# Optimization experiments

Measured on AMD Instinct MI355X. Metric: run time of the kernel, lower is better.

The kernel has to match this reference:

```python
import jax, jax.numpy as jnp
import numpy as np
from jax import lax

T, H, I, E = 1024, 1024, 512, 16          # tokens, hidden, moe_intermediate, n_routed_experts
TOP_K, N_GROUP, TOPK_GROUP = 4, 4, 2
N_SHARED = 2
I_SHARED = I * N_SHARED                    # shared-expert intermediate size
ROUTED_SCALE = 2.5


def setup_inputs() -> dict:
    key = jax.random.key(0)
    ks = jax.random.split(key, 9)
    s = lambda k, shape, fan: jax.random.normal(k, shape, jnp.float32) * (fan ** -0.5)
    return {
        "hidden_states": jax.random.normal(ks[0], (T, H), jnp.float32),
        "router_w": s(ks[1], (H, E), H),                 # gate: ReplicatedLinear(H, E)
        "e_bias": jax.random.normal(ks[2], (E,), jnp.float32) * 0.01,  # e_score_correction_bias
        "w_gate": s(ks[3], (E, H, I), H),                # routed experts gate_proj
        "w_up": s(ks[4], (E, H, I), H),                  # routed experts up_proj
        "w_down": s(ks[5], (E, I, H), I),                # routed experts down_proj
        "sw_gate": s(ks[6], (H, I_SHARED), H),           # shared experts gate_proj
        "sw_up": s(ks[7], (H, I_SHARED), H),             # shared experts up_proj
        "sw_down": s(ks[8], (I_SHARED, H), I_SHARED),    # shared experts down_proj
    }


def _grouped_topk_sigmoid(logits, e_bias):
    # DeepSeek-V3 'noaux_tc' grouped top-k with sigmoid scoring.
    scores = jax.nn.sigmoid(logits)                      # [T, E]
    sc = scores + e_bias                                 # biased scores for selection only
    g = sc.reshape(-1, N_GROUP, E // N_GROUP)
    group_scores = lax.top_k(g, 2)[0].sum(-1)            # [T, n_group]: sum of top-2 per group
    _, gidx = lax.top_k(group_scores, TOPK_GROUP)        # [T, topk_group]
    gmask = jax.nn.one_hot(gidx, N_GROUP, dtype=sc.dtype).sum(1)  # [T, n_group]
    emask = jnp.repeat(gmask, E // N_GROUP, axis=1)      # [T, E]
    masked = jnp.where(emask > 0, sc, 0.0)               # sigmoid scores are >=0
    _, tidx = lax.top_k(masked, TOP_K)                   # [T, top_k]
    w = jnp.take_along_axis(scores, tidx, axis=1)        # weights use UNbiased scores
    w = w / (w.sum(-1, keepdims=True) + 1e-20)           # norm_topk_prob=True
    # dense combine weights [T, E]
    combine = (jax.nn.one_hot(tidx, E, dtype=w.dtype) * w[..., None]).sum(1)
    return combine


def reference(hidden_states, router_w, e_bias, w_gate, w_up, w_down,
              sw_gate, sw_up, sw_down):
    x = hidden_states                                    # [T, H]
    logits = x @ router_w                                # [T, E]
    combine = _grouped_topk_sigmoid(logits, e_bias)      # [T, E]

    # routed experts: SiLU-gated MLP per expert, dense-over-experts reference
    gp = jnp.einsum('th,ehi->tei', x, w_gate)            # [T, E, I]
    up = jnp.einsum('th,ehi->tei', x, w_up)
    h = jax.nn.silu(gp) * up
    oe = jnp.einsum('tei,eih->teh', h, w_down)           # [T, E, H]
    routed = jnp.einsum('teh,te->th', oe, combine)       # [T, H]

    # shared experts MLP (reduce_results=False path), fp32 path scales routed only
    shared = (jax.nn.silu(x @ sw_gate) * (x @ sw_up)) @ sw_down  # [T, H]
    return routed * ROUTED_SCALE + shared
```

## Files before the change

### kernel.cpp

```cpp
#include <hip/hip_runtime.h>
#include <stdint.h>

#define T_TOK 1024
#define HDIM  1024
#define IDIM  512
#define NEXP  16
#define ISH   1024
#define MAXT128  48
#define HSLOTS   6144

typedef _Float16 f16;
typedef __attribute__((ext_vector_type(8))) _Float16 f16x8;
typedef __attribute__((ext_vector_type(4))) _Float16 f16x4;
typedef __attribute__((ext_vector_type(4))) float    f32x4;

__device__ __forceinline__ void gld16(const void* g, void* l) {
  __builtin_amdgcn_global_load_lds(
      (__attribute__((address_space(1))) void*)(uintptr_t)g,
      (__attribute__((address_space(3))) void*)(uint32_t)(uintptr_t)l,
      16, 0, 0);
}

__device__ __forceinline__ f16x8 ldsfragA(const f16* buf, int row, int lch) {
  int phys = lch ^ (row & 7);
  return *(const f16x8*)(buf + row * 64 + phys * 8);
}

__device__ __forceinline__ f16x8 ldsfragB(const f16* buf, int n, int kc) {
  int c = kc ^ ((n >> 3) & 7);
  return *(const f16x8*)(buf + n * 72 + c * 8);
}

__device__ __forceinline__ void stageB(const float* __restrict__ W, int ldW,
                                       int kt, int n0, f16* __restrict__ Bs,
                                       int nbase, int tid) {
  int p = tid & 31, kg = tid >> 5;
  int n = 2 * p;
  const float* src = W + (size_t)(kt + 8 * kg) * ldW + n0 + n;
  float2 v[8];
#pragma unroll
  for (int r = 0; r < 8; r++) v[r] = *(const float2*)(src + (size_t)r * ldW);
  f16x8 c0, c1;
#pragma unroll
  for (int r = 0; r < 8; r++) { c0[r] = (f16)v[r].x; c1[r] = (f16)v[r].y; }
  int nn = nbase + n;
  int cc = kg ^ ((nn >> 3) & 7);
  *(f16x8*)(Bs + (size_t)nn * 72 + cc * 8) = c0;
  *(f16x8*)(Bs + (size_t)(nn + 1) * 72 + cc * 8) = c1;
}

__global__ __launch_bounds__(256) void router_kernel(
    const float* __restrict__ x, const float* __restrict__ rw, const float* __restrict__ ebias,
    f16* __restrict__ xh, int* __restrict__ topk_i, float* __restrict__ topk_w) {
  int wave = threadIdx.x >> 6, l = threadIdx.x & 63;
  int t = blockIdx.x * 4 + wave;
  float acc[16];
#pragma unroll
  for (int e = 0; e < 16; e++) acc[e] = 0.f;
#pragma unroll
  for (int i = 0; i < 4; i++) {
    int k = i * 256 + l * 4;
    float4 xv = *(const float4*)(x + (size_t)t * HDIM + k);
    f16x4 h = { (f16)xv.x, (f16)xv.y, (f16)xv.z, (f16)xv.w };
    *(f16x4*)(xh + (size_t)t * HDIM + k) = h;
    const float* xp = &xv.x;
#pragma unroll
    for (int j = 0; j < 4; j++) {
      float xj = xp[j];
      const float4* w4 = (const float4*)(rw + (size_t)(k + j) * 16);
#pragma unroll
      for (int q = 0; q < 4; q++) {
        float4 w = w4[q];
        acc[q*4+0] += xj * w.x; acc[q*4+1] += xj * w.y;
        acc[q*4+2] += xj * w.z; acc[q*4+3] += xj * w.w;
      }
    }
  }
#pragma unroll
  for (int off = 32; off >= 1; off >>= 1)
#pragma unroll
    for (int e = 0; e < 16; e++) acc[e] += __shfl_xor(acc[e], off, 64);

  if (l == 0) {
    float s[16], sc[16];
#pragma unroll
    for (int e = 0; e < 16; e++) {
      s[e] = 1.f / (1.f + __expf(-acc[e]));
      sc[e] = s[e] + ebias[e];
    }
    float gs[4];
#pragma unroll
    for (int g = 0; g < 4; g++) {
      float a = -1e30f, b2 = -1e30f;
#pragma unroll
      for (int j = 0; j < 4; j++) {
        float v = sc[g*4 + j];
        if (v > a) { b2 = a; a = v; } else if (v > b2) { b2 = v; }
      }
      gs[g] = a + b2;
    }
    int g1 = 0;
    for (int g = 1; g < 4; g++) if (gs[g] > gs[g1]) g1 = g;
    int g2 = -1;
    for (int g = 0; g < 4; g++) if (g != g1 && (g2 < 0 || gs[g] > gs[g2])) g2 = g;
    float masked[16];
#pragma unroll
    for (int e = 0; e < 16; e++) {
      int g = e >> 2;
      masked[e] = (g == g1 || g == g2) ? sc[e] : 0.0f;
    }
    int idx[4]; float wv[4]; float denom = 1e-20f;
#pragma unroll
    for (int j = 0; j < 4; j++) {
      int best = 0; float bv = masked[0];
      for (int e = 1; e < 16; e++) if (masked[e] > bv) { bv = masked[e]; best = e; }
      idx[j] = best; wv[j] = s[best]; denom += s[best];
      masked[best] = -1e30f;
    }
#pragma unroll
    for (int j = 0; j < 4; j++) {
      topk_i[t * 4 + j] = idx[j];
      topk_w[t * 4 + j] = wv[j] / denom * 2.5f;
    }
  }
}

__global__ __launch_bounds__(1024) void scatter_kernel(
    const int* __restrict__ tki,
    int* __restrict__ tok, int* __restrict__ slotmap,
    int* __restrict__ tile_e, int* __restrict__ tile_srow,
    int* __restrict__ tile_hb, int* __restrict__ ntl) {
  __shared__ int lcnt[NEXP], lpos[NEXP], lbase[NEXP];
  int t = threadIdx.x;
  if (t < NEXP) { lcnt[t] = 0; lpos[t] = 0; }
  __syncthreads();
  int idx[4];
#pragma unroll
  for (int j = 0; j < 4; j++) idx[j] = tki[t*4+j];
#pragma unroll
  for (int j = 0; j < 4; j++) atomicAdd(&lcnt[idx[j]], 1);
  __syncthreads();
  if (t == 0) {
    int total = 0, slots = 0;
    for (int e = 0; e < NEXP; e++) {
      int c = lcnt[e], nt = (c + 127) >> 7;
      lbase[e] = slots;
      for (int j = 0; j < nt; j++) {
        tile_e[total] = e; tile_srow[total] = j * 128; tile_hb[total] = slots + j * 128; total++;
      }
      slots += nt * 128;
    }
    ntl[0] = total;
  }
  __syncthreads();
#pragma unroll
  for (int j = 0; j < 4; j++) {
    int slot = atomicAdd(&lpos[idx[j]], 1);
    tok[idx[j] * T_TOK + slot] = t;
    slotmap[t * 4 + j] = lbase[idx[j]] + slot;
  }
  __syncthreads();
  int e = t >> 6, s = t & 63;
  int c = lcnt[e];
  int top = ((c + 127) >> 7) << 7;
  for (int s2 = c + s; s2 < top; s2 += 64) tok[e * T_TOK + s2] = 0;
}

__device__ __forceinline__ f32x4 mfma16(f16x8 a, f16x8 b, f32x4 c) {
  return __builtin_amdgcn_mfma_f32_16x16x32_f16(a, b, c, 0, 0, 0);
}

__global__ __launch_bounds__(256) void gu_all(
    const f16* __restrict__ xh,
    const float* __restrict__ sg, const float* __restrict__ su, f16* __restrict__ hsh,
    const float* __restrict__ wg, const float* __restrict__ wu, f16* __restrict__ hbuf,
    const int* __restrict__ tile_e, const int* __restrict__ tile_srow,
    const int* __restrict__ tile_hb, const int* __restrict__ ntl,
    const int* __restrict__ tok) {
  int b = blockIdx.x;
  const float *Bg, *Bu; f16* Hdst;
  int e = 0, srow = 0, mbase, n0, N;
  bool gather = (b >= 128);
  if (!gather) {
    Bg = sg; Bu = su; Hdst = hsh; N = ISH;
    mbase = (b >> 4) * 128; n0 = (b & 15) * 64;
  } else {
    int rb = b - 128, by = rb >> 3;
    if (by >= ntl[0]) return;
    e = tile_e[by]; srow = tile_srow[by]; mbase = tile_hb[by];
    size_t bo = (size_t)e * HDIM * IDIM;
    Bg = wg + bo; Bu = wu + bo; Hdst = hbuf; N = IDIM;
    n0 = (rb & 7) * 64;
  }
  const int K = HDIM;

  __shared__ f16 As[128 * 64];
  __shared__ f16 Bgs[64 * 72], Bus[64 * 72];

  int tid = threadIdx.x, lane = tid & 63, wave = tid >> 6;
  int quad = lane >> 4, l15 = lane & 15;
  int r = lane >> 3, p = lane & 7;

  const f16* gbA[4]; f16* lbA[4];
#pragma unroll
  for (int jj = 0; jj < 4; jj++) {
    int j = wave * 4 + jj;
    int kcol = (p ^ r) << 3;
    int row = j * 8 + r;
    int grow = gather ? tok[e * T_TOK + srow + row] : (mbase + row);
    gbA[jj] = xh + (size_t)grow * K + kcol;
    lbA[jj] = (f16*)As + (j << 9);
  }

  int wr = wave >> 1, wc = wave & 1;
  f32x4 zero = {0.f, 0.f, 0.f, 0.f};
  f32x4 aG[4][2], aU[4][2];
#pragma unroll
  for (int mi = 0; mi < 4; mi++)
#pragma unroll
    for (int ni = 0; ni < 2; ni++) { aG[mi][ni] = zero; aU[mi][ni] = zero; }

  for (int kt = 0; kt < K; kt += 64) {
    __syncthreads();
#pragma unroll
    for (int jj = 0; jj < 4; jj++) gld16(gbA[jj] + kt, lbA[jj]);
    stageB(Bg, N, kt, n0, Bgs, 0, tid);
    stageB(Bu, N, kt, n0, Bus, 0, tid);
    __syncthreads();
#pragma unroll
    for (int ks = 0; ks < 2; ks++) {
      int lch = (ks << 2) + quad;
      f16x8 a[4], g[2], u[2];
#pragma unroll
      for (int mi = 0; mi < 4; mi++) a[mi] = ldsfragA(As, 64 * wr + 16 * mi + l15, lch);
#pragma unroll
      for (int ni = 0; ni < 2; ni++) {
        g[ni] = ldsfragB(Bgs, 32 * wc + 16 * ni + l15, lch);
        u[ni] = ldsfragB(Bus, 32 * wc + 16 * ni + l15, lch);
      }
#pragma unroll
      for (int mi = 0; mi < 4; mi++)
#pragma unroll
        for (int ni = 0; ni < 2; ni++) {
          aG[mi][ni] = mfma16(a[mi], g[ni], aG[mi][ni]);
          aU[mi][ni] = mfma16(a[mi], u[ni], aU[mi][ni]);
        }
    }
  }
#pragma unroll
  for (int mi = 0; mi < 4; mi++)
#pragma unroll
    for (int ni = 0; ni < 2; ni++)
#pragma unroll
      for (int rg = 0; rg < 4; rg++) {
        int m = 64 * wr + 16 * mi + (quad << 2) + rg;
        int n = n0 + 32 * wc + 16 * ni + l15;
        float g = aG[mi][ni][rg], u = aU[mi][ni][rg];
        float val = (g / (1.f + __expf(-g))) * u;
        Hdst[(size_t)(mbase + m) * N + n] = (f16)val;
      }
}

__global__ __launch_bounds__(256) void down_all(
    const f16* __restrict__ hsh, const float* __restrict__ sd,
    const f16* __restrict__ hbuf, const float* __restrict__ wd,
    float* __restrict__ out, f16* __restrict__ odown,
    const int* __restrict__ tile_hb, const int* __restrict__ tile_e,
    const int* __restrict__ ntl) {
  int b = blockIdx.x;
  bool routed = (b >= 64);
  const f16* A; const float* B; int K, abase, n0;
  if (!routed) {
    A = hsh; B = sd; K = ISH;
    abase = (b >> 3) * 128; n0 = (b & 7) * 128;
  } else {
    int rb = b - 64, by = rb >> 3;
    if (by >= ntl[0]) return;
    abase = tile_hb[by];
    A = hbuf; B = wd + (size_t)tile_e[by] * IDIM * HDIM; K = IDIM;
    n0 = (rb & 7) * 128;
  }

  __shared__ f16 As[128 * 64];
  __shared__ f16 Bs[128 * 72];

  int tid = threadIdx.x, lane = tid & 63, wave = tid >> 6;
  int quad = lane >> 4, l15 = lane & 15;
  int r = lane >> 3, p = lane & 7;

  const f16* gbA[4]; f16* lbA[4];
#pragma unroll
  for (int jj = 0; jj < 4; jj++) {
    int j = wave * 4 + jj;
    int kcol = (p ^ r) << 3;
    int row = j * 8 + r;
    gbA[jj] = A + (size_t)(abase + row) * K + kcol;
    lbA[jj] = (f16*)As + (j << 9);
  }

  int wr = wave >> 1, wc = wave & 1;
  f32x4 zero = {0.f, 0.f, 0.f, 0.f};
  f32x4 ac[4][4];
#pragma unroll
  for (int mi = 0; mi < 4; mi++)
#pragma unroll
    for (int ni = 0; ni < 4; ni++) ac[mi][ni] = zero;

  for (int kt = 0; kt < K; kt += 64) {
    __syncthreads();
#pragma unroll
    for (int jj = 0; jj < 4; jj++) gld16(gbA[jj] + kt, lbA[jj]);
    stageB(B, HDIM, kt, n0,      Bs, 0,  tid);
    stageB(B, HDIM, kt, n0 + 64, Bs, 64, tid);
    __syncthreads();
#pragma unroll
    for (int ks = 0; ks < 2; ks++) {
      int lch = (ks << 2) + quad;
      f16x8 a[4], bb[4];
#pragma unroll
      for (int mi = 0; mi < 4; mi++) a[mi] = ldsfragA(As, 64 * wr + 16 * mi + l15, lch);
#pragma unroll
      for (int ni = 0; ni < 4; ni++) bb[ni] = ldsfragB(Bs, 64 * wc + 16 * ni + l15, lch);
#pragma unroll
      for (int mi = 0; mi < 4; mi++)
#pragma unroll
        for (int ni = 0; ni < 4; ni++)
          ac[mi][ni] = mfma16(a[mi], bb[ni], ac[mi][ni]);
    }
  }
#pragma unroll
  for (int mi = 0; mi < 4; mi++)
#pragma unroll
    for (int ni = 0; ni < 4; ni++)
#pragma unroll
      for (int rg = 0; rg < 4; rg++) {
        int m = 64 * wr + 16 * mi + (quad << 2) + rg;
        int n = n0 + 64 * wc + 16 * ni + l15;
        if (routed) odown[(size_t)(abase + m) * HDIM + n] = (f16)ac[mi][ni][rg];
        else        out  [(size_t)(abase + m) * HDIM + n] = ac[mi][ni][rg];
      }
}

__global__ __launch_bounds__(256) void combine_kernel(
    const f16* __restrict__ odown, const int* __restrict__ slotmap,
    const float* __restrict__ tkw, float* __restrict__ out) {
  int t = blockIdx.x;
  __shared__ int ss[4]; __shared__ float sw[4];
  if (threadIdx.x < 4) {
    ss[threadIdx.x] = slotmap[t * 4 + threadIdx.x];
    sw[threadIdx.x] = tkw[t * 4 + threadIdx.x];
  }
  __syncthreads();
  int h = threadIdx.x * 4;
  float4 acc = *(const float4*)(out + (size_t)t * HDIM + h);
#pragma unroll
  for (int j = 0; j < 4; j++) {
    f16x4 v = *(const f16x4*)(odown + (size_t)ss[j] * HDIM + h);
    float wj = sw[j];
    acc.x += wj * (float)v[0]; acc.y += wj * (float)v[1];
    acc.z += wj * (float)v[2]; acc.w += wj * (float)v[3];
  }
  *(float4*)(out + (size_t)t * HDIM + h) = acc;
}

extern "C" void kernel_launch(void* const* d_in, const int* in_sizes, int n_in,
                              void* d_out, int out_size, void* d_ws, size_t ws_size,
                              hipStream_t stream) {
  const float* x  = (const float*)d_in[0];
  const float* rw = (const float*)d_in[1];
  const float* eb = (const float*)d_in[2];
  const float* wg = (const float*)d_in[3];
  const float* wu = (const float*)d_in[4];
  const float* wd = (const float*)d_in[5];
  const float* sg = (const float*)d_in[6];
  const float* su = (const float*)d_in[7];
  const float* sd = (const float*)d_in[8];
  float* out = (float*)d_out;
  (void)in_sizes; (void)n_in; (void)out_size; (void)ws_size;

  char* w = (char*)d_ws;
  size_t off = 0;
  auto alloc = [&](size_t b) { void* p = w + off; off = (off + b + 255) & ~(size_t)255; return p; };

  f16* xh   = (f16*)alloc((size_t)T_TOK * HDIM * 2);
  f16* hbuf = (f16*)alloc((size_t)HSLOTS * IDIM * 2);
  f16* hsh  = (f16*)alloc((size_t)T_TOK * ISH * 2);
  f16* odown = (f16*)alloc((size_t)HSLOTS * HDIM * 2);
  int* topk_i = (int*)alloc((size_t)T_TOK * 4 * 4);
  float* topk_w = (float*)alloc((size_t)T_TOK * 4 * 4);
  int* tok  = (int*)alloc((size_t)NEXP * T_TOK * 4);
  int* slotmap = (int*)alloc((size_t)T_TOK * 4 * 4);
  int* tile_e    = (int*)alloc(MAXT128 * 4);
  int* tile_srow = (int*)alloc(MAXT128 * 4);
  int* tile_hb   = (int*)alloc(MAXT128 * 4);
  int* ntl       = (int*)alloc(16);

  router_kernel<<<T_TOK / 4, 256, 0, stream>>>(x, rw, eb, xh, topk_i, topk_w);
  scatter_kernel<<<1, 1024, 0, stream>>>(topk_i, tok, slotmap,
                                         tile_e, tile_srow, tile_hb, ntl);
  gu_all<<<128 + MAXT128 * 8, 256, 0, stream>>>(
      xh, sg, su, hsh, wg, wu, hbuf, tile_e, tile_srow, tile_hb, ntl, tok);
  down_all<<<64 + MAXT128 * 8, 256, 0, stream>>>(
      hsh, sd, hbuf, wd, out, odown, tile_hb, tile_e, ntl);
  combine_kernel<<<T_TOK, 256, 0, stream>>>(odown, slotmap, topk_w, out);
}
```

Before: 228.0 us.

## Double-buffer GEMM K-loop and shrink tiles to raise block count

Both GEMM kernels now prefetch the next K-slice into registers (B, fp32 weights) and a second LDS buffer (A) while the current slice feeds the MFMAs. This overlaps global loads with compute instead of the previous load-sync-compute pattern. It also halves the tile sizes: gate/up goes to 64-row M tiles with matching 64-row expert tiles, and down goes to 64-column N tiles. The aim is to launch more blocks and fill more CUs. In exchange there is more redundant weight traffic per block, and the scheduler must now build two tile lists.

```diff
diff --git a/kernel.cpp b/kernel.cpp
--- a/kernel.cpp
+++ b/kernel.cpp
@@ -6,6 +6,7 @@
 #define IDIM  512
 #define NEXP  16
 #define ISH   1024
+#define MAXT64   96
 #define MAXT128  48
 #define HSLOTS   6144
 
@@ -20,33 +21,36 @@
       (__attribute__((address_space(3))) void*)(uint32_t)(uintptr_t)l,
       16, 0, 0);
 }
+__device__ __forceinline__ void barrier_raw()  { __builtin_amdgcn_s_barrier(); }
+__device__ __forceinline__ void barrier_full() {
+  __builtin_amdgcn_s_waitcnt(0);
+  __builtin_amdgcn_s_barrier();
+}
 
 __device__ __forceinline__ f16x8 ldsfragA(const f16* buf, int row, int lch) {
   int phys = lch ^ (row & 7);
   return *(const f16x8*)(buf + row * 64 + phys * 8);
 }
-
 __device__ __forceinline__ f16x8 ldsfragB(const f16* buf, int n, int kc) {
   int c = kc ^ ((n >> 3) & 7);
   return *(const f16x8*)(buf + n * 72 + c * 8);
 }
-
-__device__ __forceinline__ void stageB(const float* __restrict__ W, int ldW,
-                                       int kt, int n0, f16* __restrict__ Bs,
-                                       int nbase, int tid) {
+__device__ __forceinline__ void loadB(const float* __restrict__ W, int ldW,
+                                      int kt, int n0, int tid, float2 v[8]) {
   int p = tid & 31, kg = tid >> 5;
-  int n = 2 * p;
-  const float* src = W + (size_t)(kt + 8 * kg) * ldW + n0 + n;
-  float2 v[8];
+  const float* src = W + (size_t)(kt + 8 * kg) * ldW + n0 + 2 * p;
 #pragma unroll
   for (int r = 0; r < 8; r++) v[r] = *(const float2*)(src + (size_t)r * ldW);
+}
+__device__ __forceinline__ void writeB(const float2 v[8], f16* __restrict__ Bs, int tid) {
+  int p = tid & 31, kg = tid >> 5;
   f16x8 c0, c1;
 #pragma unroll
   for (int r = 0; r < 8; r++) { c0[r] = (f16)v[r].x; c1[r] = (f16)v[r].y; }
-  int nn = nbase + n;
+  int nn = 2 * p;
   int cc = kg ^ ((nn >> 3) & 7);
-  *(f16x8*)(Bs + (size_t)nn * 72 + cc * 8) = c0;
-  *(f16x8*)(Bs + (size_t)(nn + 1) * 72 + cc * 8) = c1;
+  *(f16x8*)(Bs + nn * 72 + cc * 8) = c0;
+  *(f16x8*)(Bs + (nn + 1) * 72 + cc * 8) = c1;
 }
 
 __global__ __launch_bounds__(256) void router_kernel(
@@ -128,8 +132,9 @@
 __global__ __launch_bounds__(1024) void scatter_kernel(
     const int* __restrict__ tki,
     int* __restrict__ tok, int* __restrict__ slotmap,
-    int* __restrict__ tile_e, int* __restrict__ tile_srow,
-    int* __restrict__ tile_hb, int* __restrict__ ntl) {
+    int* __restrict__ t64_e, int* __restrict__ t64_srow, int* __restrict__ t64_hb,
+    int* __restrict__ t128_e, int* __restrict__ t128_srow, int* __restrict__ t128_hb,
+    int* __restrict__ ntl) {
   __shared__ int lcnt[NEXP], lpos[NEXP], lbase[NEXP];
   int t = threadIdx.x;
   if (t < NEXP) { lcnt[t] = 0; lpos[t] = 0; }
@@ -141,16 +146,19 @@
   for (int j = 0; j < 4; j++) atomicAdd(&lcnt[idx[j]], 1);
   __syncthreads();
   if (t == 0) {
-    int total = 0, slots = 0;
+    int n64 = 0, n128 = 0, slots = 0;
     for (int e = 0; e < NEXP; e++) {
-      int c = lcnt[e], nt = (c + 127) >> 7;
+      int c = lcnt[e], top = ((c + 127) >> 7) << 7;
       lbase[e] = slots;
-      for (int j = 0; j < nt; j++) {
-        tile_e[total] = e; tile_srow[total] = j * 128; tile_hb[total] = slots + j * 128; total++;
-      }
-      slots += nt * 128;
-    }
-    ntl[0] = total;
+      for (int j = 0; j < top / 64; j++) {
+        t64_e[n64] = e; t64_srow[n64] = j * 64; t64_hb[n64] = slots + j * 64; n64++;
+      }
+      for (int j = 0; j < top / 128; j++) {
+        t128_e[n128] = e; t128_srow[n128] = j * 128; t128_hb[n128] = slots + j * 128; n128++;
+      }
+      slots += top;
+    }
+    ntl[0] = n64; ntl[1] = n128;
   }
   __syncthreads();
 #pragma unroll
@@ -174,86 +182,102 @@
     const f16* __restrict__ xh,
     const float* __restrict__ sg, const float* __restrict__ su, f16* __restrict__ hsh,
     const float* __restrict__ wg, const float* __restrict__ wu, f16* __restrict__ hbuf,
-    const int* __restrict__ tile_e, const int* __restrict__ tile_srow,
-    const int* __restrict__ tile_hb, const int* __restrict__ ntl,
+    const int* __restrict__ t64_e, const int* __restrict__ t64_srow,
+    const int* __restrict__ t64_hb, const int* __restrict__ ntl,
     const int* __restrict__ tok) {
   int b = blockIdx.x;
   const float *Bg, *Bu; f16* Hdst;
   int e = 0, srow = 0, mbase, n0, N;
-  bool gather = (b >= 128);
+  bool gather = (b >= 256);
   if (!gather) {
     Bg = sg; Bu = su; Hdst = hsh; N = ISH;
-    mbase = (b >> 4) * 128; n0 = (b & 15) * 64;
+    mbase = (b >> 4) * 64; n0 = (b & 15) * 64;
   } else {
-    int rb = b - 128, by = rb >> 3;
+    int rb = b - 256, by = rb >> 3;
     if (by >= ntl[0]) return;
-    e = tile_e[by]; srow = tile_srow[by]; mbase = tile_hb[by];
+    e = t64_e[by]; srow = t64_srow[by]; mbase = t64_hb[by];
     size_t bo = (size_t)e * HDIM * IDIM;
     Bg = wg + bo; Bu = wu + bo; Hdst = hbuf; N = IDIM;
     n0 = (rb & 7) * 64;
   }
-  const int K = HDIM;
-
-  __shared__ f16 As[128 * 64];
+  const int K = HDIM, nk = HDIM / 64;
+
+  __shared__ f16 As[2][64 * 64];
   __shared__ f16 Bgs[64 * 72], Bus[64 * 72];
 
   int tid = threadIdx.x, lane = tid & 63, wave = tid >> 6;
   int quad = lane >> 4, l15 = lane & 15;
   int r = lane >> 3, p = lane & 7;
 
-  const f16* gbA[4]; f16* lbA[4];
-#pragma unroll
-  for (int jj = 0; jj < 4; jj++) {
-    int j = wave * 4 + jj;
+  const f16* gbA[2]; int lofA[2];
+#pragma unroll
+  for (int jj = 0; jj < 2; jj++) {
+    int j = wave * 2 + jj;
     int kcol = (p ^ r) << 3;
     int row = j * 8 + r;
     int grow = gather ? tok[e * T_TOK + srow + row] : (mbase + row);
     gbA[jj] = xh + (size_t)grow * K + kcol;
-    lbA[jj] = (f16*)As + (j << 9);
+    lofA[jj] = j << 9;
   }
 
   int wr = wave >> 1, wc = wave & 1;
   f32x4 zero = {0.f, 0.f, 0.f, 0.f};
-  f32x4 aG[4][2], aU[4][2];
-#pragma unroll
-  for (int mi = 0; mi < 4; mi++)
+  f32x4 aG[2][2], aU[2][2];
+#pragma unroll
+  for (int mi = 0; mi < 2; mi++)
 #pragma unroll
     for (int ni = 0; ni < 2; ni++) { aG[mi][ni] = zero; aU[mi][ni] = zero; }
 
-  for (int kt = 0; kt < K; kt += 64) {
-    __syncthreads();
-#pragma unroll
-    for (int jj = 0; jj < 4; jj++) gld16(gbA[jj] + kt, lbA[jj]);
-    stageB(Bg, N, kt, n0, Bgs, 0, tid);
-    stageB(Bu, N, kt, n0, Bus, 0, tid);
-    __syncthreads();
+  float2 vg[8], vu[8];
+  loadB(Bg, N, 0, n0, tid, vg);
+  loadB(Bu, N, 0, n0, tid, vu);
+#pragma unroll
+  for (int jj = 0; jj < 2; jj++) gld16(gbA[jj], (f16*)As[0] + lofA[jj]);
+  writeB(vg, Bgs, tid);
+  writeB(vu, Bus, tid);
+  barrier_full();
+
+  for (int kt = 0; kt < nk; kt++) {
+    int cur = kt & 1;
+    bool more = (kt + 1 < nk);
+    if (more) {
+      loadB(Bg, N, (kt + 1) * 64, n0, tid, vg);
+      loadB(Bu, N, (kt + 1) * 64, n0, tid, vu);
+#pragma unroll
+      for (int jj = 0; jj < 2; jj++)
+        gld16(gbA[jj] + (kt + 1) * 64, (f16*)As[1 - cur] + lofA[jj]);
+    }
+    const f16* Ac = As[cur];
 #pragma unroll
     for (int ks = 0; ks < 2; ks++) {
       int lch = (ks << 2) + quad;
-      f16x8 a[4], g[2], u[2];
-#pragma unroll
-      for (int mi = 0; mi < 4; mi++) a[mi] = ldsfragA(As, 64 * wr + 16 * mi + l15, lch);
+      f16x8 a[2], g[2], u[2];
+#pragma unroll
+      for (int mi = 0; mi < 2; mi++) a[mi] = ldsfragA(Ac, 32 * wr + 16 * mi + l15, lch);
 #pragma unroll
       for (int ni = 0; ni < 2; ni++) {
         g[ni] = ldsfragB(Bgs, 32 * wc + 16 * ni + l15, lch);
         u[ni] = ldsfragB(Bus, 32 * wc + 16 * ni + l15, lch);
       }
 #pragma unroll
-      for (int mi = 0; mi < 4; mi++)
+      for (int mi = 0; mi < 2; mi++)
 #pragma unroll
         for (int ni = 0; ni < 2; ni++) {
           aG[mi][ni] = mfma16(a[mi], g[ni], aG[mi][ni]);
           aU[mi][ni] = mfma16(a[mi], u[ni], aU[mi][ni]);
         }
     }
-  }
-#pragma unroll
-  for (int mi = 0; mi < 4; mi++)
+    barrier_raw();
+    if (more) { writeB(vg, Bgs, tid); writeB(vu, Bus, tid); }
+    barrier_full();
+  }
+#pragma unroll
+  for (int mi = 0; mi < 2; mi++)
 #pragma unroll
     for (int ni = 0; ni < 2; ni++)
 #pragma unroll
       for (int rg = 0; rg < 4; rg++) {
-        int m = 64 * wr + 16 * mi + (quad << 2) + rg;
+        int m = 32 * wr + 16 * mi + (quad << 2) + rg;
         int n = n0 + 32 * wc + 16 * ni + l15;
         float g = aG[mi][ni][rg], u = aU[mi][ni][rg];
         float val = (g / (1.f + __expf(-g))) * u;
@@ -265,77 +289,91 @@
     const f16* __restrict__ hsh, const float* __restrict__ sd,
     const f16* __restrict__ hbuf, const float* __restrict__ wd,
     float* __restrict__ out, f16* __restrict__ odown,
-    const int* __restrict__ tile_hb, const int* __restrict__ tile_e,
+    const int* __restrict__ t128_e, const int* __restrict__ t128_hb,
     const int* __restrict__ ntl) {
   int b = blockIdx.x;
-  bool routed = (b >= 64);
+  bool routed = (b >= 128);
   const f16* A; const float* B; int K, abase, n0;
   if (!routed) {
     A = hsh; B = sd; K = ISH;
-    abase = (b >> 3) * 128; n0 = (b & 7) * 128;
+    abase = (b >> 4) * 128; n0 = (b & 15) * 64;
   } else {
-    int rb = b - 64, by = rb >> 3;
-    if (by >= ntl[0]) return;
-    abase = tile_hb[by];
-    A = hbuf; B = wd + (size_t)tile_e[by] * IDIM * HDIM; K = IDIM;
-    n0 = (rb & 7) * 128;
-  }
-
-  __shared__ f16 As[128 * 64];
-  __shared__ f16 Bs[128 * 72];
+    int rb = b - 128, by = rb >> 4;
+    if (by >= ntl[1]) return;
+    abase = t128_hb[by];
+    A = hbuf; B = wd + (size_t)t128_e[by] * IDIM * HDIM; K = IDIM;
+    n0 = (rb & 15) * 64;
+  }
+  const int nk = K / 64;
+
+  __shared__ f16 As[2][128 * 64];
+  __shared__ f16 Bs[64 * 72];
 
   int tid = threadIdx.x, lane = tid & 63, wave = tid >> 6;
   int quad = lane >> 4, l15 = lane & 15;
   int r = lane >> 3, p = lane & 7;
 
-  const f16* gbA[4]; f16* lbA[4];
+  const f16* gbA[4]; int lofA[4];
 #pragma unroll
   for (int jj = 0; jj < 4; jj++) {
     int j = wave * 4 + jj;
     int kcol = (p ^ r) << 3;
     int row = j * 8 + r;
     gbA[jj] = A + (size_t)(abase + row) * K + kcol;
-    lbA[jj] = (f16*)As + (j << 9);
+    lofA[jj] = j << 9;
   }
 
   int wr = wave >> 1, wc = wave & 1;
   f32x4 zero = {0.f, 0.f, 0.f, 0.f};
-  f32x4 ac[4][4];
+  f32x4 ac[4][2];
 #pragma unroll
   for (int mi = 0; mi < 4; mi++)
 #pragma unroll
-    for (int ni = 0; ni < 4; ni++) ac[mi][ni] = zero;
-
-  for (int kt = 0; kt < K; kt += 64) {
-    __syncthreads();
-#pragma unroll
-    for (int jj = 0; jj < 4; jj++) gld16(gbA[jj] + kt, lbA[jj]);
-    stageB(B, HDIM, kt, n0,      Bs, 0,  tid);
-    stageB(B, HDIM, kt, n0 + 64, Bs, 64, tid);
-    __syncthreads();
+    for (int ni = 0; ni < 2; ni++) ac[mi][ni] = zero;
+
+  float2 vb[8];
+  loadB(B, HDIM, 0, n0, tid, vb);
+#pragma unroll
+  for (int jj = 0; jj < 4; jj++) gld16(gbA[jj], (f16*)As[0] + lofA[jj]);
+  writeB(vb, Bs, tid);
+  barrier_full();
+
+  for (int kt = 0; kt < nk; kt++) {
+    int cur = kt & 1;
+    bool more = (kt + 1 < nk);
+    if (more) {
+      loadB(B, HDIM, (kt + 1) * 64, n0, tid, vb);
+#pragma unroll
+      for (int jj = 0; jj < 4; jj++)
+        gld16(gbA[jj] + (kt + 1) * 64, (f16*)As[1 - cur] + lofA[jj]);
+    }
+    const f16* Ac = As[cur];
 #pragma unroll
     for (int ks = 0; ks < 2; ks++) {
       int lch = (ks << 2) + quad;
-      f16x8 a[4], bb[4];
-#pragma unroll
-      for (int mi = 0; mi < 4; mi++) a[mi] = ldsfragA(As, 64 * wr + 16 * mi + l15, lch);
-#pragma unroll
-      for (int ni = 0; ni < 4; ni++) bb[ni] = ldsfragB(Bs, 64 * wc + 16 * ni + l15, lch);
+      f16x8 a[4], bb[2];
+#pragma unroll
+      for (int mi = 0; mi < 4; mi++) a[mi] = ldsfragA(Ac, 64 * wr + 16 * mi + l15, lch);
+#pragma unroll
+      for (int ni = 0; ni < 2; ni++) bb[ni] = ldsfragB(Bs, 32 * wc + 16 * ni + l15, lch);
 #pragma unroll
       for (int mi = 0; mi < 4; mi++)
 #pragma unroll
-        for (int ni = 0; ni < 4; ni++)
+        for (int ni = 0; ni < 2; ni++)
           ac[mi][ni] = mfma16(a[mi], bb[ni], ac[mi][ni]);
     }
+    barrier_raw();
+    if (more) writeB(vb, Bs, tid);
+    barrier_full();
   }
 #pragma unroll
   for (int mi = 0; mi < 4; mi++)
 #pragma unroll
-    for (int ni = 0; ni < 4; ni++)
+    for (int ni = 0; ni < 2; ni++)
 #pragma unroll
       for (int rg = 0; rg < 4; rg++) {
         int m = 64 * wr + 16 * mi + (quad << 2) + rg;
-        int n = n0 + 64 * wc + 16 * ni + l15;
+        int n = n0 + 32 * wc + 16 * ni + l15;
         if (routed) odown[(size_t)(abase + m) * HDIM + n] = (f16)ac[mi][ni][rg];
         else        out  [(size_t)(abase + m) * HDIM + n] = ac[mi][ni][rg];
       }
@@ -390,17 +428,21 @@
   float* topk_w = (float*)alloc((size_t)T_TOK * 4 * 4);
   int* tok  = (int*)alloc((size_t)NEXP * T_TOK * 4);
   int* slotmap = (int*)alloc((size_t)T_TOK * 4 * 4);
-  int* tile_e    = (int*)alloc(MAXT128 * 4);
-  int* tile_srow = (int*)alloc(MAXT128 * 4);
-  int* tile_hb   = (int*)alloc(MAXT128 * 4);
-  int* ntl       = (int*)alloc(16);
+  int* t64_e  = (int*)alloc(MAXT64 * 4);
+  int* t64_sr = (int*)alloc(MAXT64 * 4);
+  int* t64_hb = (int*)alloc(MAXT64 * 4);
+  int* t128_e  = (int*)alloc(MAXT128 * 4);
+  int* t128_sr = (int*)alloc(MAXT128 * 4);
+  int* t128_hb = (int*)alloc(MAXT128 * 4);
+  int* ntl     = (int*)alloc(16);
 
   router_kernel<<<T_TOK / 4, 256, 0, stream>>>(x, rw, eb, xh, topk_i, topk_w);
   scatter_kernel<<<1, 1024, 0, stream>>>(topk_i, tok, slotmap,
-                                         tile_e, tile_srow, tile_hb, ntl);
-  gu_all<<<128 + MAXT128 * 8, 256, 0, stream>>>(
-      xh, sg, su, hsh, wg, wu, hbuf, tile_e, tile_srow, tile_hb, ntl, tok);
-  down_all<<<64 + MAXT128 * 8, 256, 0, stream>>>(
-      hsh, sd, hbuf, wd, out, odown, tile_hb, tile_e, ntl);
+                                         t64_e, t64_sr, t64_hb,
+                                         t128_e, t128_sr, t128_hb, ntl);
+  gu_all<<<256 + MAXT64 * 8, 256, 0, stream>>>(
+      xh, sg, su, hsh, wg, wu, hbuf, t64_e, t64_sr, t64_hb, ntl, tok);
+  down_all<<<128 + MAXT128 * 16, 256, 0, stream>>>(
+      hsh, sd, hbuf, wd, out, odown, t128_e, t128_hb, ntl);
   combine_kernel<<<T_TOK, 256, 0, stream>>>(odown, slotmap, topk_w, out);
 }
```

After: 242.4 us. 1.06x slower.
